# Kernel optimization log

Hardware: AMD Instinct MI355X
Metric: run time of the kernel (lower is better)

The kernel has to match this reference:

```python
import jax, jax.numpy as jnp
import numpy as np

N = 50000
E = 1600000
IN_CH = 128
HID = 32
HEADS = 4
OUT_CH = 64
NEG_SLOPE = 0.2


def _seg_softmax(e, seg, n):
    # e: [E,H], seg: [E] destination indices -> per-destination softmax
    m = jax.ops.segment_max(e, seg, num_segments=n)          # [N,H]
    ex = jnp.exp(e - m[seg])
    s = jax.ops.segment_sum(ex, seg, num_segments=n)         # [N,H]
    return ex / (s[seg] + 1e-16)


def _gat_conv(x, edge_index, W, a_src, a_dst, b, concat):
    # x: [N,Fin]; W: [Fin, H*C]; a_src/a_dst: [H,C]; b: [H*C] or [C]
    H, C = a_src.shape
    n = x.shape[0]
    h = (x @ W).reshape(n, H, C)                              # [N,H,C]
    src, dst = edge_index[0], edge_index[1]
    as_ = jnp.einsum('nhc,hc->nh', h, a_src)                  # [N,H]
    ad_ = jnp.einsum('nhc,hc->nh', h, a_dst)
    e = jax.nn.leaky_relu(as_[src] + ad_[dst], NEG_SLOPE)     # [E,H]
    alpha = _seg_softmax(e, dst, n)                           # [E,H]
    msg = h[src] * alpha[:, :, None]                          # [E,H,C]
    out = jax.ops.segment_sum(msg, dst, num_segments=n)       # [N,H,C]
    out = out.reshape(n, H * C) if concat else out.mean(axis=1)
    return out + b, alpha


def _layer_norm(x, w, b, eps=1e-5):
    mu = x.mean(-1, keepdims=True)
    var = x.var(-1, keepdims=True)
    return (x - mu) * jax.lax.rsqrt(var + eps) * w + b


def setup_inputs() -> dict:
    key = jax.random.key(0)
    ks = jax.random.split(key, 20)
    g = lambda k, s: jax.random.normal(k, s, dtype=jnp.float32) * 0.05
    d = {
        'x': jax.random.normal(ks[0], (N, IN_CH), dtype=jnp.float32),
        'edge_index': jax.random.randint(ks[1], (2, E), 0, N, dtype=jnp.int64),
        # gat1: in=IN_CH, out=HID, heads, concat
        'W1': g(ks[2], (IN_CH, HEADS * HID)),
        'a_src1': g(ks[3], (HEADS, HID)),
        'a_dst1': g(ks[4], (HEADS, HID)),
        'b1': jnp.zeros((HEADS * HID,), jnp.float32),
        'ln1_w': jnp.ones((HEADS * HID,), jnp.float32),
        'ln1_b': jnp.zeros((HEADS * HID,), jnp.float32),
        'Wskip': g(ks[5], (IN_CH, HEADS * HID)),
        'bskip': jnp.zeros((HEADS * HID,), jnp.float32),
        # gat2: in=HEADS*HID, out=HID, concat
        'W2': g(ks[6], (HEADS * HID, HEADS * HID)),
        'a_src2': g(ks[7], (HEADS, HID)),
        'a_dst2': g(ks[8], (HEADS, HID)),
        'b2': jnp.zeros((HEADS * HID,), jnp.float32),
        'ln2_w': jnp.ones((HEADS * HID,), jnp.float32),
        'ln2_b': jnp.zeros((HEADS * HID,), jnp.float32),
        # gat3: in=HEADS*HID, out=OUT_CH, concat=False (mean over heads)
        'W3': g(ks[9], (HEADS * HID, HEADS * OUT_CH)),
        'a_src3': g(ks[10], (HEADS, OUT_CH)),
        'a_dst3': g(ks[11], (HEADS, OUT_CH)),
        'b3': jnp.zeros((OUT_CH,), jnp.float32),
    }
    return d


def reference(x, edge_index, W1, a_src1, a_dst1, b1, ln1_w, ln1_b,
              Wskip, bskip, W2, a_src2, a_dst2, b2, ln2_w, ln2_b,
              W3, a_src3, a_dst3, b3):
    x_skip = x
    h, alpha1 = _gat_conv(x, edge_index, W1, a_src1, a_dst1, b1, concat=True)
    h = jax.nn.elu(h)
    h = _layer_norm(h, ln1_w, ln1_b)
    h = h + (x_skip @ Wskip + bskip)
    h, alpha2 = _gat_conv(h, edge_index, W2, a_src2, a_dst2, b2, concat=True)
    h = jax.nn.elu(h)
    h = _layer_norm(h, ln2_w, ln2_b)
    out, alpha3 = _gat_conv(h, edge_index, W3, a_src3, a_dst3, b3, concat=False)
    return out, alpha1, alpha2, alpha3
```

## Files before the change

### kernel.cpp

```cpp
#include <hip/hip_runtime.h>

#define NN 50000
#define EE 1600000
#define SCAN_B 196
#define NB 196
#define CHUNK 2048
#define G1 782
#define L1 (NB * G1)
#define B1 599

typedef __attribute__((ext_vector_type(8))) short bf16x8;
typedef __attribute__((ext_vector_type(4))) float f32x4;
typedef __attribute__((ext_vector_type(2))) float f32x2;

#if __has_builtin(__builtin_elementwise_fma)
#define PKFMA(a, b, c) __builtin_elementwise_fma((a), (b), (c))
#else
#define PKFMA(a, b, c) ((a) * (b) + (c))
#endif

__device__ __forceinline__ float bfu(unsigned short u) { return __uint_as_float((unsigned)u << 16); }
__device__ __forceinline__ float bflo(unsigned u) { return __uint_as_float(u << 16); }
__device__ __forceinline__ float bfhi(unsigned u) { return __uint_as_float(u & 0xffff0000u); }
__device__ __forceinline__ f32x2 bfpk(unsigned u) {
    f32x2 r; r.x = bflo(u); r.y = bfhi(u); return r;
}
__device__ __forceinline__ unsigned short f2bf(float f) {
    unsigned u = __float_as_uint(f);
    u += 0x7fff + ((u >> 16) & 1);
    return (unsigned short)(u >> 16);
}
__device__ __forceinline__ unsigned pk2(float a, float b) {
    return (unsigned)f2bf(a) | ((unsigned)f2bf(b) << 16);
}
__device__ __forceinline__ float cvt_load(const void* p, int i, bool f32) {
    if (f32) return ((const float*)p)[i];
    return bfu(((const unsigned short*)p)[i]);
}

__global__ void detect_k(const void* ei_raw, const void* x_raw, int* flags) {
    __shared__ int s_i64, s_f32;
    const int t = threadIdx.x;
    if (t == 0) { s_i64 = 1; s_f32 = 0; }
    __syncthreads();
    const int* ei32 = (const int*)ei_raw;
    if (ei32[2 * t + 1] != 0) atomicAnd(&s_i64, 0);
    const unsigned short* xu = (const unsigned short*)x_raw;
    int found = 0;
    for (int j = 0; j < 32; j++) {
        unsigned short u = xu[t * 32 + j];
        if ((u & 0x7F80) == 0x7F80) found = 1;
    }
    if (found) atomicOr(&s_f32, 1);
    __syncthreads();
    if (t == 0) { flags[0] = s_i64; flags[1] = s_f32; }
}

__global__ __launch_bounds__(256) void hist1_k(const void* ei_raw, const int* flags,
                                               int2* __restrict__ edges, int* __restrict__ cnt)
{
    __shared__ int h[NB];
    const int t = threadIdx.x;
    const int i64 = __builtin_amdgcn_readfirstlane(flags[0]);
    if (t < NB) h[t] = 0;
    __syncthreads();
    const int beg = blockIdx.x * CHUNK;
    const int end = min(beg + CHUNK, EE);
    for (int e = beg + t; e < end; e += 256) {
        int2 v;
        if (i64) { const long long* p = (const long long*)ei_raw; v.x = (int)p[e]; v.y = (int)p[EE + e]; }
        else     { const int* p = (const int*)ei_raw;             v.x = p[e];      v.y = p[EE + e];      }
        edges[e] = v;
        atomicAdd(&h[v.y >> 8], 1);
    }
    __syncthreads();
    if (t < NB) cnt[(size_t)t * G1 + blockIdx.x] = h[t];
}

__global__ __launch_bounds__(256) void scanAg_k(int* __restrict__ cnt, int* __restrict__ bsum2) {
    __shared__ int ps[256];
    const int b = blockIdx.x, t = threadIdx.x;
    const int i = b * 256 + t;
    const int v = (i < L1) ? cnt[i] : 0;
    ps[t] = v;
    __syncthreads();
    for (int off = 1; off < 256; off <<= 1) {
        const int u = (t >= off) ? ps[t - off] : 0;
        __syncthreads();
        ps[t] += u;
        __syncthreads();
    }
    if (i < L1) cnt[i] = ps[t] - v;
    if (t == 255) bsum2[b] = ps[255];
}
__global__ void scanBg_k(int* bsum2) {
    __shared__ int ps[256];
    const int t = threadIdx.x;
    int vals[3];
    int s = 0;
    #pragma unroll
    for (int i = 0; i < 3; i++) {
        const int idx = t * 3 + i;
        vals[i] = (idx < B1) ? bsum2[idx] : 0;
        s += vals[i];
    }
    ps[t] = s;
    __syncthreads();
    for (int off = 1; off < 256; off <<= 1) {
        const int u = (t >= off) ? ps[t - off] : 0;
        __syncthreads();
        ps[t] += u;
        __syncthreads();
    }
    int run = t ? ps[t - 1] : 0;
    #pragma unroll
    for (int i = 0; i < 3; i++) {
        const int idx = t * 3 + i;
        if (idx < B1) bsum2[idx] = run;
        run += vals[i];
    }
}
__global__ __launch_bounds__(256) void scanCg_k(int* __restrict__ cnt, const int* __restrict__ bsum2,
                                                int* __restrict__ bstart) {
    const int i = blockIdx.x * 256 + threadIdx.x;
    if (i < L1) {
        const int r = cnt[i] + bsum2[blockIdx.x];
        cnt[i] = r;
        if (i % G1 == 0) bstart[i / G1] = r;
    }
    if (i == 0) bstart[NB] = EE;
}

__global__ __launch_bounds__(256) void scatter_k(const int2* __restrict__ edges,
                                                 const int* __restrict__ cnt,
                                                 int2* __restrict__ bedges)
{
    __shared__ int ofs[NB];
    const int t = threadIdx.x;
    if (t < NB) ofs[t] = cnt[(size_t)t * G1 + blockIdx.x];
    __syncthreads();
    const int beg = blockIdx.x * CHUNK;
    const int end = min(beg + CHUNK, EE);
    for (int e = beg + t; e < end; e += 256) {
        const int2 v = edges[e];
        const int p = atomicAdd(&ofs[v.y >> 8], 1);
        bedges[p] = v;
    }
}

__global__ __launch_bounds__(256) void hist_k(const int2* __restrict__ bedges,
                                              const int* __restrict__ bstart, int* __restrict__ deg)
{
    __shared__ int h[256];
    const int b = blockIdx.x, t = threadIdx.x;
    h[t] = 0;
    __syncthreads();
    const int lo = bstart[b], hi = bstart[b + 1];
    for (int i = lo + t; i < hi; i += 256)
        atomicAdd(&h[bedges[i].y & 255], 1);
    __syncthreads();
    const int d = b * 256 + t;
    if (d < NN) deg[d] = h[t];
}

__global__ __launch_bounds__(256) void scanA_k(const int* __restrict__ deg,
                                               int* __restrict__ roff, int* __restrict__ bsum) {
    __shared__ int ps[256];
    const int b = blockIdx.x, t = threadIdx.x;
    const int i = b * 256 + t;
    const int v = (i < NN) ? deg[i] : 0;
    ps[t] = v;
    __syncthreads();
    for (int off = 1; off < 256; off <<= 1) {
        const int u = (t >= off) ? ps[t - off] : 0;
        __syncthreads();
        ps[t] += u;
        __syncthreads();
    }
    if (i < NN) roff[i] = ps[t] - v;
    if (t == 255) bsum[b] = ps[255];
}
__global__ void scanB_k(int* bsum) {
    __shared__ int ps[256];
    const int t = threadIdx.x;
    const int v = (t < SCAN_B) ? bsum[t] : 0;
    ps[t] = v;
    __syncthreads();
    for (int off = 1; off < 256; off <<= 1) {
        const int u = (t >= off) ? ps[t - off] : 0;
        __syncthreads();
        ps[t] += u;
        __syncthreads();
    }
    if (t < SCAN_B) bsum[t] = ps[t] - v;
}
__global__ __launch_bounds__(256) void scanC_k(int* __restrict__ roff, const int* __restrict__ bsum) {
    const int b = blockIdx.x, t = threadIdx.x;
    const int i = b * 256 + t;
    if (i < NN) roff[i] += bsum[b];
}

__global__ __launch_bounds__(256) void place_k(const int2* __restrict__ bedges,
                                               const int* __restrict__ bstart, const int* __restrict__ roff,
                                               int* __restrict__ csrc)
{
    __shared__ int cur[256];
    const int b = blockIdx.x, t = threadIdx.x;
    const int d = b * 256 + t;
    cur[t] = (d < NN) ? roff[d] : 0;
    __syncthreads();
    const int lo = bstart[b], hi = bstart[b + 1];
    for (int i = lo + t; i < hi; i += 256) {
        const int2 v = bedges[i];
        const int p = atomicAdd(&cur[v.y & 255], 1);
        csrc[p] = v.x;
    }
}

__global__ __launch_bounds__(256) void cvt_all_k(
    const void* x, const void* W1, const void* Wskip, const void* W2, const void* W3,
    const void* as1, const void* ad1, const void* b1, const void* l1w, const void* l1b,
    const void* bsk, const void* as2, const void* ad2, const void* b2, const void* l2w,
    const void* l2b, const void* as3, const void* ad3, const void* b3,
    unsigned short* xb, unsigned short* Wt1, unsigned short* Wts, unsigned short* Wt2,
    unsigned short* Wt3, float* smalls, const int* flags)
{
    const bool f32 = __builtin_amdgcn_readfirstlane(flags[1]) != 0;
    const int gid = blockIdx.x * 256 + threadIdx.x;
    if (gid < NN * 128) { xb[gid] = f2bf(cvt_load(x, gid, f32)); return; }
    int g = gid - NN * 128;
    if (g < 16384) { Wt1[g] = f2bf(cvt_load(W1,    (g & 127) * 128 + (g >> 7), f32)); return; }
    g -= 16384;
    if (g < 16384) { Wts[g] = f2bf(cvt_load(Wskip, (g & 127) * 128 + (g >> 7), f32)); return; }
    g -= 16384;
    if (g < 16384) { Wt2[g] = f2bf(cvt_load(W2,    (g & 127) * 128 + (g >> 7), f32)); return; }
    g -= 16384;
    if (g < 32768) { Wt3[g] = f2bf(cvt_load(W3,    (g & 127) * 256 + (g >> 7), f32)); return; }
    g -= 32768;
    if (g >= 2432) return;
    const void* src; int off;
    if      (g < 128)  { src = as1; off = g;        }
    else if (g < 256)  { src = ad1; off = g - 128;  }
    else if (g < 384)  { src = b1;  off = g - 256;  }
    else if (g < 512)  { src = l1w; off = g - 384;  }
    else if (g < 640)  { src = l1b; off = g - 512;  }
    else if (g < 768)  { src = bsk; off = g - 640;  }
    else if (g < 896)  { src = as2; off = g - 768;  }
    else if (g < 1024) { src = ad2; off = g - 896;  }
    else if (g < 1152) { src = b2;  off = g - 1024; }
    else if (g < 1280) { src = l2w; off = g - 1152; }
    else if (g < 1408) { src = l2b; off = g - 1280; }
    else if (g < 1664) { src = as3; off = g - 1408; }
    else if (g < 1920) { src = ad3; off = g - 1664; }
    else               { src = b3;  off = g - 1920; }
    smalls[g] = cvt_load(src, off, f32);
}

__global__ void prep_v_k(const unsigned short* __restrict__ Wt3, const float* __restrict__ as3,
                         const float* __restrict__ ad3, float* __restrict__ vsrc, float* __restrict__ vdst)
{
    const int t = blockIdx.x * 256 + threadIdx.x;
    if (t >= 512) return;
    const int h = t >> 7, k = t & 127;
    float ss = 0.f, dd = 0.f;
    for (int c = 0; c < 64; c++) {
        const float w = bfu(Wt3[(size_t)(h * 64 + c) * 128 + k]);
        ss = fmaf(w, as3[h * 64 + c], ss);
        dd = fmaf(w, ad3[h * 64 + c], dd);
    }
    vsrc[t] = ss; vdst[t] = dd;
}

template<int FOUT, bool DOTS>
__global__ __launch_bounds__(256) void mfma_mm_k(
    const unsigned short* __restrict__ Xb, const unsigned short* __restrict__ Wt,
    unsigned short* __restrict__ Hb,
    const float* __restrict__ asrc, const float* __restrict__ adst,
    float* __restrict__ as_, float* __restrict__ dpk)
{
    constexpr int NT = FOUT / 16;
    const int tile = blockIdx.x * 4 + (threadIdx.x >> 6);
    if (tile >= 3125) return;
    const int l = threadIdx.x & 63;
    const int lr = l & 15, lq = l >> 4;
    const int m0 = tile * 16;
    f32x4 acc[NT];
    #pragma unroll
    for (int nt = 0; nt < NT; nt++) { acc[nt][0]=0.f; acc[nt][1]=0.f; acc[nt][2]=0.f; acc[nt][3]=0.f; }
    #pragma unroll
    for (int kb = 0; kb < 4; kb++) {
        const bf16x8 a = *(const bf16x8*)(Xb + (size_t)(m0 + lr) * 128 + kb * 32 + lq * 8);
        #pragma unroll
        for (int nt = 0; nt < NT; nt++) {
            const bf16x8 b = *(const bf16x8*)(Wt + (size_t)(nt * 16 + lr) * 128 + kb * 32 + lq * 8);
            acc[nt] = __builtin_amdgcn_mfma_f32_16x16x32_bf16(a, b, acc[nt], 0, 0, 0);
        }
    }
    #pragma unroll
    for (int nt = 0; nt < NT; nt++)
        #pragma unroll
        for (int r = 0; r < 4; r++)
            Hb[(size_t)(m0 + lq * 4 + r) * FOUT + nt * 16 + lr] = f2bf(acc[nt][r]);
    if (DOTS) {
        #pragma unroll
        for (int hd = 0; hd < 4; hd++) {
            const float a0 = asrc[hd * 32 + lr], a1 = asrc[hd * 32 + 16 + lr];
            const float d0 = adst[hd * 32 + lr], d1 = adst[hd * 32 + 16 + lr];
            #pragma unroll
            for (int r = 0; r < 4; r++) {
                float ps = acc[2 * hd][r] * a0 + acc[2 * hd + 1][r] * a1;
                float pd = acc[2 * hd][r] * d0 + acc[2 * hd + 1][r] * d1;
                #pragma unroll
                for (int m = 8; m; m >>= 1) { ps += __shfl_xor(ps, m); pd += __shfl_xor(pd, m); }
                if (lr == 0) {
                    const int node = m0 + lq * 4 + r;
                    as_[(size_t)node * 4 + hd] = ps;
                    dpk[(size_t)node * 8 + hd] = pd;
                }
            }
        }
    }
}

__global__ __launch_bounds__(256) void mm12_k(
    const unsigned short* __restrict__ Xb, const unsigned short* __restrict__ Wt1,
    unsigned short* __restrict__ Hb, unsigned short* __restrict__ Sb,
    const float* __restrict__ asrc, const float* __restrict__ adst,
    float* __restrict__ as_, float* __restrict__ dpk)
{
    const int tile = blockIdx.x * 4 + (threadIdx.x >> 6);
    if (tile >= 3125) return;
    const int l = threadIdx.x & 63;
    const int lr = l & 15, lq = l >> 4;
    const int m0 = tile * 16;
    f32x4 acc[16];
    #pragma unroll
    for (int nt = 0; nt < 16; nt++) { acc[nt][0]=0.f; acc[nt][1]=0.f; acc[nt][2]=0.f; acc[nt][3]=0.f; }
    #pragma unroll
    for (int kb = 0; kb < 4; kb++) {
        const bf16x8 a = *(const bf16x8*)(Xb + (size_t)(m0 + lr) * 128 + kb * 32 + lq * 8);
        #pragma unroll
        for (int nt = 0; nt < 16; nt++) {
            const bf16x8 b = *(const bf16x8*)(Wt1 + (size_t)(nt * 16 + lr) * 128 + kb * 32 + lq * 8);
            acc[nt] = __builtin_amdgcn_mfma_f32_16x16x32_bf16(a, b, acc[nt], 0, 0, 0);
        }
    }
    #pragma unroll
    for (int nt = 0; nt < 8; nt++)
        #pragma unroll
        for (int r = 0; r < 4; r++)
            Hb[(size_t)(m0 + lq * 4 + r) * 128 + nt * 16 + lr] = f2bf(acc[nt][r]);
    #pragma unroll
    for (int nt = 8; nt < 16; nt++)
        #pragma unroll
        for (int r = 0; r < 4; r++)
            Sb[(size_t)(m0 + lq * 4 + r) * 128 + (nt - 8) * 16 + lr] = f2bf(acc[nt][r]);
    #pragma unroll
    for (int hd = 0; hd < 4; hd++) {
        const float a0 = asrc[hd * 32 + lr], a1 = asrc[hd * 32 + 16 + lr];
        const float d0 = adst[hd * 32 + lr], d1 = adst[hd * 32 + 16 + lr];
        #pragma unroll
        for (int r = 0; r < 4; r++) {
            float ps = acc[2 * hd][r] * a0 + acc[2 * hd + 1][r] * a1;
            float pd = acc[2 * hd][r] * d0 + acc[2 * hd + 1][r] * d1;
            #pragma unroll
            for (int m = 8; m; m >>= 1) { ps += __shfl_xor(ps, m); pd += __shfl_xor(pd, m); }
            if (lr == 0) {
                const int node = m0 + lq * 4 + r;
                as_[(size_t)node * 4 + hd] = ps;
                dpk[(size_t)node * 8 + hd] = pd;
            }
        }
    }
}

__device__ __forceinline__ float4 edge_w(float4 as4, float4 ad4) {
    float4 e4;
    e4.x = as4.x + ad4.x; e4.y = as4.y + ad4.y; e4.z = as4.z + ad4.z; e4.w = as4.w + ad4.w;
    e4.x = e4.x >= 0.f ? e4.x : 0.2f * e4.x;
    e4.y = e4.y >= 0.f ? e4.y : 0.2f * e4.y;
    e4.z = e4.z >= 0.f ? e4.z : 0.2f * e4.z;
    e4.w = e4.w >= 0.f ? e4.w : 0.2f * e4.w;
    float4 w4;
    w4.x = __expf(e4.x); w4.y = __expf(e4.y); w4.z = __expf(e4.z); w4.w = __expf(e4.w);
    return w4;
}

template<bool HAS_SKIP, bool DOTS3>
__global__ __launch_bounds__(256) void fagg12_k(
    const int* __restrict__ roff, const int* __restrict__ deg,
    const int* __restrict__ csrc, const float* __restrict__ as_, float* __restrict__ dpk,
    const unsigned short* __restrict__ Hb,
    const float* __restrict__ b, const float* __restrict__ lnw, const float* __restrict__ lnb,
    const unsigned short* __restrict__ skipb, const float* __restrict__ bskip,
    unsigned short* __restrict__ xoutb,
    const float* __restrict__ vsrc, const float* __restrict__ vdst,
    float* __restrict__ as3o, float* __restrict__ dpk3o)
{
    __shared__ float lws[4][512];
    const int warp = threadIdx.x >> 6;
    const int lane = threadIdx.x & 63;
    const int node = blockIdx.x * 4 + warp;
    const int q = lane & 15, g = lane >> 4;
    const int h = q >> 2;
    float* lw = lws[warp];
    const int ro = roff[node], dg = deg[node];
    const float4 ad4 = *(const float4*)(dpk + (size_t)node * 8);

    float4 sv = make_float4(0.f, 0.f, 0.f, 0.f);
    f32x2 acc2[4];
    #pragma unroll
    for (int i = 0; i < 4; i++) { acc2[i].x = 0.f; acc2[i].y = 0.f; }

    for (int j0 = 0; j0 < dg; j0 += 64) {
        const int jn = min(64, dg - j0);
        int src = 0;
        float4 w4 = make_float4(0.f, 0.f, 0.f, 0.f);
        if (lane < jn) {
            src = csrc[ro + j0 + lane];
            const float4 as4 = *(const float4*)(as_ + (size_t)src * 4);
            w4 = edge_w(as4, ad4);
            sv.x += w4.x; sv.y += w4.y; sv.z += w4.z; sv.w += w4.w;
        }
        const float sf = __int_as_float(src);
        *(float4*)(lw + lane * 8)     = make_float4(w4.x, sf, w4.y, sf);
        *(float4*)(lw + lane * 8 + 4) = make_float4(w4.z, sf, w4.w, sf);
        const int jq = (jn + 3) >> 2;
        #pragma unroll 2
        for (int j = 0; j < jq; j++) {
            const int e = 4 * j + g;
            const float2 rd = *(const float2*)(lw + e * 8 + h * 2);
            f32x2 ww; ww.x = rd.x; ww.y = rd.x;
            const unsigned soff = (__float_as_uint(rd.y) << 8) + (unsigned)(q << 4);
            const uint4 hv = *(const uint4*)((const char*)Hb + soff);
            acc2[0] = PKFMA(ww, bfpk(hv.x), acc2[0]);
            acc2[1] = PKFMA(ww, bfpk(hv.y), acc2[1]);
            acc2[2] = PKFMA(ww, bfpk(hv.z), acc2[2]);
            acc2[3] = PKFMA(ww, bfpk(hv.w), acc2[3]);
        }
    }

    #pragma unroll
    for (int i = 0; i < 4; i++) {
        acc2[i].x += __shfl_xor(acc2[i].x, 16);
        acc2[i].y += __shfl_xor(acc2[i].y, 16);
        acc2[i].x += __shfl_xor(acc2[i].x, 32);
        acc2[i].y += __shfl_xor(acc2[i].y, 32);
    }
    #pragma unroll
    for (int m = 32; m; m >>= 1) {
        sv.x += __shfl_xor(sv.x, m); sv.y += __shfl_xor(sv.y, m);
        sv.z += __shfl_xor(sv.z, m); sv.w += __shfl_xor(sv.w, m);
    }
    float4 rs;
    rs.x = 1.f / (sv.x + 1e-16f); rs.y = 1.f / (sv.y + 1e-16f);
    rs.z = 1.f / (sv.z + 1e-16f); rs.w = 1.f / (sv.w + 1e-16f);
    if (lane == 0) *(float4*)(dpk + (size_t)node * 8 + 4) = rs;
    const float rsh = (h == 0) ? rs.x : (h == 1) ? rs.y : (h == 2) ? rs.z : rs.w;

    const float4 b0 = *(const float4*)(b + q * 8);
    const float4 b1 = *(const float4*)(b + q * 8 + 4);
    float v[8];
    v[0] = acc2[0].x * rsh + b0.x; v[1] = acc2[0].y * rsh + b0.y;
    v[2] = acc2[1].x * rsh + b0.z; v[3] = acc2[1].y * rsh + b0.w;
    v[4] = acc2[2].x * rsh + b1.x; v[5] = acc2[2].y * rsh + b1.y;
    v[6] = acc2[3].x * rsh + b1.z; v[7] = acc2[3].y * rsh + b1.w;
    float s1 = 0.f, s2 = 0.f;
    #pragma unroll
    for (int i = 0; i < 8; i++) {
        v[i] = v[i] > 0.f ? v[i] : expm1f(v[i]);
        s1 += v[i]; s2 += v[i] * v[i];
    }
    #pragma unroll
    for (int m = 8; m; m >>= 1) { s1 += __shfl_xor(s1, m); s2 += __shfl_xor(s2, m); }
    const float mu   = s1 * (1.f / 128.f);
    const float var  = s2 * (1.f / 128.f) - mu * mu;
    const float rstd = rsqrtf(var + 1e-5f);
    const float4 w0 = *(const float4*)(lnw + q * 8);
    const float4 w1 = *(const float4*)(lnw + q * 8 + 4);
    const float4 o0 = *(const float4*)(lnb + q * 8);
    const float4 o1 = *(const float4*)(lnb + q * 8 + 4);
    float y[8];
    y[0] = (v[0] - mu) * rstd * w0.x + o0.x; y[1] = (v[1] - mu) * rstd * w0.y + o0.y;
    y[2] = (v[2] - mu) * rstd * w0.z + o0.z; y[3] = (v[3] - mu) * rstd * w0.w + o0.w;
    y[4] = (v[4] - mu) * rstd * w1.x + o1.x; y[5] = (v[5] - mu) * rstd * w1.y + o1.y;
    y[6] = (v[6] - mu) * rstd * w1.z + o1.z; y[7] = (v[7] - mu) * rstd * w1.w + o1.w;
    if (HAS_SKIP) {
        const uint4 sk = *(const uint4*)(skipb + (size_t)node * 128 + q * 8);
        const float4 k0 = *(const float4*)(bskip + q * 8);
        const float4 k1 = *(const float4*)(bskip + q * 8 + 4);
        y[0] += bflo(sk.x) + k0.x; y[1] += bfhi(sk.x) + k0.y;
        y[2] += bflo(sk.y) + k0.z; y[3] += bfhi(sk.y) + k0.w;
        y[4] += bflo(sk.z) + k1.x; y[5] += bfhi(sk.z) + k1.y;
        y[6] += bflo(sk.w) + k1.z; y[7] += bfhi(sk.w) + k1.w;
    }
    if (g == 0) {
        uint4 pk;
        pk.x = pk2(y[0], y[1]); pk.y = pk2(y[2], y[3]);
        pk.z = pk2(y[4], y[5]); pk.w = pk2(y[6], y[7]);
        *(uint4*)(xoutb + (size_t)node * 128 + q * 8) = pk;
    }
    if (DOTS3) {
        #pragma unroll
        for (int hd = 0; hd < 4; hd++) {
            const float4 vs0 = *(const float4*)(vsrc + hd * 128 + q * 8);
            const float4 vs1 = *(const float4*)(vsrc + hd * 128 + q * 8 + 4);
            const float4 vd0 = *(const float4*)(vdst + hd * 128 + q * 8);
            const float4 vd1 = *(const float4*)(vdst + hd * 128 + q * 8 + 4);
            float ss = y[0] * vs0.x + y[1] * vs0.y + y[2] * vs0.z + y[3] * vs0.w
                     + y[4] * vs1.x + y[5] * vs1.y + y[6] * vs1.z + y[7] * vs1.w;
            float dd = y[0] * vd0.x + y[1] * vd0.y + y[2] * vd0.z + y[3] * vd0.w
                     + y[4] * vd1.x + y[5] * vd1.y + y[6] * vd1.z + y[7] * vd1.w;
            #pragma unroll
            for (int m = 8; m; m >>= 1) { ss += __shfl_xor(ss, m); dd += __shfl_xor(dd, m); }
            if (lane == 0) {
                as3o[(size_t)node * 4 + hd] = ss;
                dpk3o[(size_t)node * 8 + hd] = dd;
            }
        }
    }
}

__global__ __launch_bounds__(256) void fagg3_k(
    const int* __restrict__ roff, const int* __restrict__ deg,
    const int* __restrict__ csrc, const float* __restrict__ as_, float* __restrict__ dpk,
    const unsigned short* __restrict__ Xb,
    unsigned short* __restrict__ gout)
{
    __shared__ float lws[4][256];
    __shared__ int lss[4][64];
    const int warp = threadIdx.x >> 6;
    const int lane = threadIdx.x & 63;
    const int node = blockIdx.x * 4 + warp;
    const int q = lane & 31, g = lane >> 5;
    float* lw = lws[warp];
    int*   ls = lss[warp];
    const int ro = roff[node], dg = deg[node];
    const float4 ad4 = *(const float4*)(dpk + (size_t)node * 8);

    float4 sv = make_float4(0.f, 0.f, 0.f, 0.f);
    f32x2 acc2[4][2];
    #pragma unroll
    for (int hh = 0; hh < 4; hh++)
        #pragma unroll
        for (int i = 0; i < 2; i++) { acc2[hh][i].x = 0.f; acc2[hh][i].y = 0.f; }

    for (int j0 = 0; j0 < dg; j0 += 64) {
        const int jn = min(64, dg - j0);
        int src = 0;
        float4 w4 = make_float4(0.f, 0.f, 0.f, 0.f);
        if (lane < jn) {
            src = csrc[ro + j0 + lane];
            const float4 as4 = *(const float4*)(as_ + (size_t)src * 4);
            w4 = edge_w(as4, ad4);
            sv.x += w4.x; sv.y += w4.y; sv.z += w4.z; sv.w += w4.w;
        }
        *(float4*)(lw + lane * 4) = w4;
        ls[lane] = src;
        const int jq = (jn + 1) >> 1;
        #pragma unroll 2
        for (int j = 0; j < jq; j++) {
            const int e = 2 * j + g;
            const float4 w = *(const float4*)(lw + e * 4);
            const int s_ = ls[e];
            const unsigned soff = ((unsigned)s_ << 8) + (unsigned)(q << 3);
            const uint2 hv = *(const uint2*)((const char*)Xb + soff);
            const f32x2 x01 = bfpk(hv.x), x23 = bfpk(hv.y);
            f32x2 w0; w0.x = w.x; w0.y = w.x;
            f32x2 w1; w1.x = w.y; w1.y = w.y;
            f32x2 w2; w2.x = w.z; w2.y = w.z;
            f32x2 w3; w3.x = w.w; w3.y = w.w;
            acc2[0][0] = PKFMA(w0, x01, acc2[0][0]); acc2[0][1] = PKFMA(w0, x23, acc2[0][1]);
            acc2[1][0] = PKFMA(w1, x01, acc2[1][0]); acc2[1][1] = PKFMA(w1, x23, acc2[1][1]);
            acc2[2][0] = PKFMA(w2, x01, acc2[2][0]); acc2[2][1] = PKFMA(w2, x23, acc2[2][1]);
            acc2[3][0] = PKFMA(w3, x01, acc2[3][0]); acc2[3][1] = PKFMA(w3, x23, acc2[3][1]);
        }
    }

    #pragma unroll
    for (int hh = 0; hh < 4; hh++)
        #pragma unroll
        for (int i = 0; i < 2; i++) {
            acc2[hh][i].x += __shfl_xor(acc2[hh][i].x, 32);
            acc2[hh][i].y += __shfl_xor(acc2[hh][i].y, 32);
        }
    #pragma unroll
    for (int m = 32; m; m >>= 1) {
        sv.x += __shfl_xor(sv.x, m); sv.y += __shfl_xor(sv.y, m);
        sv.z += __shfl_xor(sv.z, m); sv.w += __shfl_xor(sv.w, m);
    }
    float4 rs;
    rs.x = 1.f / (sv.x + 1e-16f); rs.y = 1.f / (sv.y + 1e-16f);
    rs.z = 1.f / (sv.z + 1e-16f); rs.w = 1.f / (sv.w + 1e-16f);
    if (lane == 0) *(float4*)(dpk + (size_t)node * 8 + 4) = rs;

    unsigned short* gr = gout + (size_t)node * 512 + 4 * q;
    if (g == 0) {
        uint2 p0, p1;
        p0.x = pk2(acc2[0][0].x * rs.x, acc2[0][0].y * rs.x);
        p0.y = pk2(acc2[0][1].x * rs.x, acc2[0][1].y * rs.x);
        p1.x = pk2(acc2[1][0].x * rs.y, acc2[1][0].y * rs.y);
        p1.y = pk2(acc2[1][1].x * rs.y, acc2[1][1].y * rs.y);
        *(uint2*)(gr)       = p0;
        *(uint2*)(gr + 128) = p1;
    } else {
        uint2 p2, p3;
        p2.x = pk2(acc2[2][0].x * rs.z, acc2[2][0].y * rs.z);
        p2.y = pk2(acc2[2][1].x * rs.z, acc2[2][1].y * rs.z);
        p3.x = pk2(acc2[3][0].x * rs.w, acc2[3][0].y * rs.w);
        p3.y = pk2(acc2[3][1].x * rs.w, acc2[3][1].y * rs.w);
        *(uint2*)(gr + 256) = p2;
        *(uint2*)(gr + 384) = p3;
    }
}

__global__ __launch_bounds__(256) void alpha_l_k(
    const int2* __restrict__ edges, const float* __restrict__ as_,
    const float* __restrict__ dpk, float* __restrict__ al)
{
    const int e = blockIdx.x * 256 + threadIdx.x;
    const int2 v = edges[e];
    const float4 as4 = *(const float4*)(as_ + (size_t)v.x * 4);
    const float4 ad4 = *(const float4*)(dpk + (size_t)v.y * 8);
    const float4 r   = *(const float4*)(dpk + (size_t)v.y * 8 + 4);
    const float4 w = edge_w(as4, ad4);
    float4 a; a.x = w.x * r.x; a.y = w.y * r.y; a.z = w.z * r.z; a.w = w.w * r.w;
    *(float4*)(al + (size_t)e * 4) = a;
}

__global__ __launch_bounds__(256) void proj3_k(
    const unsigned short* __restrict__ Gb, const unsigned short* __restrict__ Wt3,
    const float* __restrict__ b3, float* __restrict__ out)
{
    const int tile = blockIdx.x * 4 + (threadIdx.x >> 6);
    if (tile >= 3125) return;
    const int l = threadIdx.x & 63;
    const int lr = l & 15, lq = l >> 4;
    const int m0 = tile * 16;
    f32x4 acc[4];
    #pragma unroll
    for (int nt = 0; nt < 4; nt++) { acc[nt][0]=0.f; acc[nt][1]=0.f; acc[nt][2]=0.f; acc[nt][3]=0.f; }
    #pragma unroll
    for (int kb = 0; kb < 16; kb++) {
        const int h = kb >> 2;
        const int kk = (kb & 3) * 32 + lq * 8;
        const bf16x8 a = *(const bf16x8*)(Gb + (size_t)(m0 + lr) * 512 + kb * 32 + lq * 8);
        #pragma unroll
        for (int nt = 0; nt < 4; nt++) {
            const int c = nt * 16 + lr;
            const bf16x8 b = *(const bf16x8*)(Wt3 + (size_t)(h * 64 + c) * 128 + kk);
            acc[nt] = __builtin_amdgcn_mfma_f32_16x16x32_bf16(a, b, acc[nt], 0, 0, 0);
        }
    }
    #pragma unroll
    for (int nt = 0; nt < 4; nt++)
        #pragma unroll
        for (int r = 0; r < 4; r++) {
            const int col = nt * 16 + lr;
            out[(size_t)(m0 + lq * 4 + r) * 64 + col] = 0.25f * acc[nt][r] + b3[col];
        }
}

extern "C" void kernel_launch(void* const* d_in, const int* in_sizes, int n_in,
                              void* d_out, int out_size, void* d_ws, size_t ws_size,
                              hipStream_t stream)
{
    char* ws = (char*)d_ws;
    unsigned short* g_bf    = (unsigned short*)(ws);
    int2*           bedges  = (int2*)(ws);
    int*            csrc    = (int*)(ws + 51200000);
    unsigned short* x_bf    = (unsigned short*)(ws + 57600000);
    unsigned short* xcur_bf = (unsigned short*)(ws + 70400000);
    unsigned short* skip_bf = (unsigned short*)(ws + 83200000);
    unsigned short* Hbuf    = (unsigned short*)(ws + 96000000);
    int2*  edges  = (int2*)(ws + 108800000);
    float* as1b   = (float*)(ws + 121600000);
    float* as2b   = as1b + 200000;
    float* as3b   = as1b + 400000;
    float* dpk1   = as1b + 600000;
    float* dpk2   = as1b + 1000000;
    float* dpk3   = as1b + 1400000;
    int*   roff   = (int*)(ws + 128800000);
    int*   deg    = (int*)(ws + 129000000);
    int*   bsum   = (int*)(ws + 129200000);
    int*   flags  = (int*)(ws + 129402048);
    unsigned short* Wt1 = (unsigned short*)(ws + 129500000);
    unsigned short* Wts = Wt1 + 16384;
    unsigned short* Wt2 = Wts + 16384;
    unsigned short* Wt3 = Wt2 + 16384;
    float* smalls = (float*)(ws + 129700000);
    float* vsrc   = (float*)(ws + 129720000);
    float* vdst   = (float*)(ws + 129730000);
    int*   cnt    = (int*)(ws + 130000000);
    int*   bsum2  = (int*)(ws + 130700000);
    int*   bstart = (int*)(ws + 130710000);

    float* as1c = smalls;          float* ad1c = smalls + 128;
    float* b1c  = smalls + 256;    float* l1wc = smalls + 384;
    float* l1bc = smalls + 512;    float* bskc = smalls + 640;
    float* as2c = smalls + 768;    float* ad2c = smalls + 896;
    float* b2c  = smalls + 1024;   float* l2wc = smalls + 1152;
    float* l2bc = smalls + 1280;   float* as3c = smalls + 1408;
    float* ad3c = smalls + 1664;   float* b3c  = smalls + 1920;

    float* out = (float*)d_out;
    float* al1 = out + (size_t)NN * 64;
    float* al2 = al1 + (size_t)EE * 4;
    float* al3 = al2 + (size_t)EE * 4;

    detect_k<<<1, 256, 0, stream>>>(d_in[1], d_in[0], flags);
    hist1_k<<<G1, 256, 0, stream>>>(d_in[1], flags, edges, cnt);
    cvt_all_k<<<25330, 256, 0, stream>>>(
        d_in[0], d_in[2], d_in[8], d_in[10], d_in[16],
        d_in[3], d_in[4], d_in[5], d_in[6], d_in[7],
        d_in[9], d_in[11], d_in[12], d_in[13], d_in[14], d_in[15],
        d_in[17], d_in[18], d_in[19],
        x_bf, Wt1, Wts, Wt2, Wt3, smalls, flags);
    scanAg_k<<<B1, 256, 0, stream>>>(cnt, bsum2);
    scanBg_k<<<1, 256, 0, stream>>>(bsum2);
    scanCg_k<<<B1, 256, 0, stream>>>(cnt, bsum2, bstart);
    scatter_k<<<G1, 256, 0, stream>>>(edges, cnt, bedges);
    hist_k<<<NB, 256, 0, stream>>>(bedges, bstart, deg);
    scanA_k<<<SCAN_B, 256, 0, stream>>>(deg, roff, bsum);
    scanB_k<<<1, 256, 0, stream>>>(bsum);
    scanC_k<<<SCAN_B, 256, 0, stream>>>(roff, bsum);
    place_k<<<NB, 256, 0, stream>>>(bedges, bstart, roff, csrc);
    prep_v_k<<<2, 256, 0, stream>>>(Wt3, as3c, ad3c, vsrc, vdst);

    mm12_k<<<782, 256, 0, stream>>>(x_bf, Wt1, Hbuf, skip_bf, as1c, ad1c, as1b, dpk1);
    fagg12_k<true, false><<<12500, 256, 0, stream>>>(roff, deg, csrc, as1b, dpk1, Hbuf,
                                                     b1c, l1wc, l1bc, skip_bf, bskc, xcur_bf,
                                                     nullptr, nullptr, nullptr, nullptr);

    mfma_mm_k<128, true><<<782, 256, 0, stream>>>(xcur_bf, Wt2, Hbuf, as2c, ad2c, as2b, dpk2);
    fagg12_k<false, true><<<12500, 256, 0, stream>>>(roff, deg, csrc, as2b, dpk2, Hbuf,
                                                     b2c, l2wc, l2bc, nullptr, nullptr, xcur_bf,
                                                     vsrc, vdst, as3b, dpk3);

    fagg3_k<<<12500, 256, 0, stream>>>(roff, deg, csrc, as3b, dpk3, xcur_bf, g_bf);
    proj3_k<<<782, 256, 0, stream>>>(g_bf, Wt3, b3c, out);

    alpha_l_k<<<6250, 256, 0, stream>>>(edges, as1b, dpk1, al1);
    alpha_l_k<<<6250, 256, 0, stream>>>(edges, as2b, dpk2, al2);
    alpha_l_k<<<6250, 256, 0, stream>>>(edges, as3b, dpk3, al3);
}
```

Before: 580.2 us.

## Process two destination nodes per wavefront in aggregation kernels

The three aggregation kernels now split each 64-lane wavefront into two 32-lane halves, each handling its own destination node. Edge chunks shrink to 32 and the grid is halved. With an average degree of about 32, fewer lanes sit idle and the cross-half shuffle reductions disappear. The ELU also swaps expm1f for __expf minus one, which trades a little accuracy near zero for cheaper math.

```diff
diff --git a/kernel.cpp b/kernel.cpp
--- a/kernel.cpp
+++ b/kernel.cpp
@@ -400,10 +400,12 @@
     __shared__ float lws[4][512];
     const int warp = threadIdx.x >> 6;
     const int lane = threadIdx.x & 63;
-    const int node = blockIdx.x * 4 + warp;
-    const int q = lane & 15, g = lane >> 4;
+    const int half = lane >> 5;
+    const int l32  = lane & 31;
+    const int node = blockIdx.x * 8 + warp * 2 + half;
+    const int q = l32 & 15, g = l32 >> 4;
     const int h = q >> 2;
-    float* lw = lws[warp];
+    float* lw = lws[warp] + half * 256;
     const int ro = roff[node], dg = deg[node];
     const float4 ad4 = *(const float4*)(dpk + (size_t)node * 8);
 
@@ -412,23 +414,23 @@
     #pragma unroll
     for (int i = 0; i < 4; i++) { acc2[i].x = 0.f; acc2[i].y = 0.f; }
 
-    for (int j0 = 0; j0 < dg; j0 += 64) {
-        const int jn = min(64, dg - j0);
+    for (int j0 = 0; j0 < dg; j0 += 32) {
+        const int jn = min(32, dg - j0);
         int src = 0;
         float4 w4 = make_float4(0.f, 0.f, 0.f, 0.f);
-        if (lane < jn) {
-            src = csrc[ro + j0 + lane];
+        if (l32 < jn) {
+            src = csrc[ro + j0 + l32];
             const float4 as4 = *(const float4*)(as_ + (size_t)src * 4);
             w4 = edge_w(as4, ad4);
             sv.x += w4.x; sv.y += w4.y; sv.z += w4.z; sv.w += w4.w;
         }
         const float sf = __int_as_float(src);
-        *(float4*)(lw + lane * 8)     = make_float4(w4.x, sf, w4.y, sf);
-        *(float4*)(lw + lane * 8 + 4) = make_float4(w4.z, sf, w4.w, sf);
-        const int jq = (jn + 3) >> 2;
+        *(float4*)(lw + l32 * 8)     = make_float4(w4.x, sf, w4.y, sf);
+        *(float4*)(lw + l32 * 8 + 4) = make_float4(w4.z, sf, w4.w, sf);
+        const int jq = (jn + 1) >> 1;
         #pragma unroll 2
         for (int j = 0; j < jq; j++) {
-            const int e = 4 * j + g;
+            const int e = 2 * j + g;
             const float2 rd = *(const float2*)(lw + e * 8 + h * 2);
             f32x2 ww; ww.x = rd.x; ww.y = rd.x;
             const unsigned soff = (__float_as_uint(rd.y) << 8) + (unsigned)(q << 4);
@@ -444,18 +446,16 @@
     for (int i = 0; i < 4; i++) {
         acc2[i].x += __shfl_xor(acc2[i].x, 16);
         acc2[i].y += __shfl_xor(acc2[i].y, 16);
-        acc2[i].x += __shfl_xor(acc2[i].x, 32);
-        acc2[i].y += __shfl_xor(acc2[i].y, 32);
-    }
-    #pragma unroll
-    for (int m = 32; m; m >>= 1) {
+    }
+    #pragma unroll
+    for (int m = 16; m; m >>= 1) {
         sv.x += __shfl_xor(sv.x, m); sv.y += __shfl_xor(sv.y, m);
         sv.z += __shfl_xor(sv.z, m); sv.w += __shfl_xor(sv.w, m);
     }
     float4 rs;
     rs.x = 1.f / (sv.x + 1e-16f); rs.y = 1.f / (sv.y + 1e-16f);
     rs.z = 1.f / (sv.z + 1e-16f); rs.w = 1.f / (sv.w + 1e-16f);
-    if (lane == 0) *(float4*)(dpk + (size_t)node * 8 + 4) = rs;
+    if (l32 == 0) *(float4*)(dpk + (size_t)node * 8 + 4) = rs;
     const float rsh = (h == 0) ? rs.x : (h == 1) ? rs.y : (h == 2) ? rs.z : rs.w;
 
     const float4 b0 = *(const float4*)(b + q * 8);
@@ -468,7 +468,7 @@
     float s1 = 0.f, s2 = 0.f;
     #pragma unroll
     for (int i = 0; i < 8; i++) {
-        v[i] = v[i] > 0.f ? v[i] : expm1f(v[i]);
+        v[i] = v[i] > 0.f ? v[i] : (__expf(v[i]) - 1.f);
         s1 += v[i]; s2 += v[i] * v[i];
     }
     #pragma unroll
@@ -513,7 +513,7 @@
                      + y[4] * vd1.x + y[5] * vd1.y + y[6] * vd1.z + y[7] * vd1.w;
             #pragma unroll
             for (int m = 8; m; m >>= 1) { ss += __shfl_xor(ss, m); dd += __shfl_xor(dd, m); }
-            if (lane == 0) {
+            if (l32 == 0) {
                 as3o[(size_t)node * 4 + hd] = ss;
                 dpk3o[(size_t)node * 8 + hd] = dd;
             }
@@ -531,10 +531,11 @@
     __shared__ int lss[4][64];
     const int warp = threadIdx.x >> 6;
     const int lane = threadIdx.x & 63;
-    const int node = blockIdx.x * 4 + warp;
-    const int q = lane & 31, g = lane >> 5;
-    float* lw = lws[warp];
-    int*   ls = lss[warp];
+    const int half = lane >> 5;
+    const int l32  = lane & 31;
+    const int node = blockIdx.x * 8 + warp * 2 + half;
+    float* lw = lws[warp] + half * 128;
+    int*   ls = lss[warp] + half * 32;
     const int ro = roff[node], dg = deg[node];
     const float4 ad4 = *(const float4*)(dpk + (size_t)node * 8);
 
@@ -545,25 +546,22 @@
         #pragma unroll
         for (int i = 0; i < 2; i++) { acc2[hh][i].x = 0.f; acc2[hh][i].y = 0.f; }
 
-    for (int j0 = 0; j0 < dg; j0 += 64) {
-        const int jn = min(64, dg - j0);
+    for (int j0 = 0; j0 < dg; j0 += 32) {
+        const int jn = min(32, dg - j0);
         int src = 0;
         float4 w4 = make_float4(0.f, 0.f, 0.f, 0.f);
-        if (lane < jn) {
-            src = csrc[ro + j0 + lane];
+        if (l32 < jn) {
+            src = csrc[ro + j0 + l32];
             const float4 as4 = *(const float4*)(as_ + (size_t)src * 4);
             w4 = edge_w(as4, ad4);
             sv.x += w4.x; sv.y += w4.y; sv.z += w4.z; sv.w += w4.w;
         }
-        *(float4*)(lw + lane * 4) = w4;
-        ls[lane] = src;
-        const int jq = (jn + 1) >> 1;
-        #pragma unroll 2
-        for (int j = 0; j < jq; j++) {
-            const int e = 2 * j + g;
-            const float4 w = *(const float4*)(lw + e * 4);
-            const int s_ = ls[e];
-            const unsigned soff = ((unsigned)s_ << 8) + (unsigned)(q << 3);
+        *(float4*)(lw + l32 * 4) = w4;
+        ls[l32] = src;
+        for (int j = 0; j < jn; j++) {
+            const float4 w = *(const float4*)(lw + j * 4);
+            const int s_ = ls[j];
+            const unsigned soff = ((unsigned)s_ << 8) + (unsigned)(l32 << 3);
             const uint2 hv = *(const uint2*)((const char*)Xb + soff);
             const f32x2 x01 = bfpk(hv.x), x23 = bfpk(hv.y);
             f32x2 w0; w0.x = w.x; w0.y = w.x;
@@ -578,40 +576,29 @@
     }
 
     #pragma unroll
-    for (int hh = 0; hh < 4; hh++)
-        #pragma unroll
-        for (int i = 0; i < 2; i++) {
-            acc2[hh][i].x += __shfl_xor(acc2[hh][i].x, 32);
-            acc2[hh][i].y += __shfl_xor(acc2[hh][i].y, 32);
-        }
-    #pragma unroll
-    for (int m = 32; m; m >>= 1) {
+    for (int m = 16; m; m >>= 1) {
         sv.x += __shfl_xor(sv.x, m); sv.y += __shfl_xor(sv.y, m);
         sv.z += __shfl_xor(sv.z, m); sv.w += __shfl_xor(sv.w, m);
     }
     float4 rs;
     rs.x = 1.f / (sv.x + 1e-16f); rs.y = 1.f / (sv.y + 1e-16f);
     rs.z = 1.f / (sv.z + 1e-16f); rs.w = 1.f / (sv.w + 1e-16f);
-    if (lane == 0) *(float4*)(dpk + (size_t)node * 8 + 4) = rs;
-
-    unsigned short* gr = gout + (size_t)node * 512 + 4 * q;
-    if (g == 0) {
-        uint2 p0, p1;
-        p0.x = pk2(acc2[0][0].x * rs.x, acc2[0][0].y * rs.x);
-        p0.y = pk2(acc2[0][1].x * rs.x, acc2[0][1].y * rs.x);
-        p1.x = pk2(acc2[1][0].x * rs.y, acc2[1][0].y * rs.y);
-        p1.y = pk2(acc2[1][1].x * rs.y, acc2[1][1].y * rs.y);
-        *(uint2*)(gr)       = p0;
-        *(uint2*)(gr + 128) = p1;
-    } else {
-        uint2 p2, p3;
-        p2.x = pk2(acc2[2][0].x * rs.z, acc2[2][0].y * rs.z);
-        p2.y = pk2(acc2[2][1].x * rs.z, acc2[2][1].y * rs.z);
-        p3.x = pk2(acc2[3][0].x * rs.w, acc2[3][0].y * rs.w);
-        p3.y = pk2(acc2[3][1].x * rs.w, acc2[3][1].y * rs.w);
-        *(uint2*)(gr + 256) = p2;
-        *(uint2*)(gr + 384) = p3;
-    }
+    if (l32 == 0) *(float4*)(dpk + (size_t)node * 8 + 4) = rs;
+
+    unsigned short* gr = gout + (size_t)node * 512 + 4 * l32;
+    uint2 p0, p1, p2, p3;
+    p0.x = pk2(acc2[0][0].x * rs.x, acc2[0][0].y * rs.x);
+    p0.y = pk2(acc2[0][1].x * rs.x, acc2[0][1].y * rs.x);
+    p1.x = pk2(acc2[1][0].x * rs.y, acc2[1][0].y * rs.y);
+    p1.y = pk2(acc2[1][1].x * rs.y, acc2[1][1].y * rs.y);
+    p2.x = pk2(acc2[2][0].x * rs.z, acc2[2][0].y * rs.z);
+    p2.y = pk2(acc2[2][1].x * rs.z, acc2[2][1].y * rs.z);
+    p3.x = pk2(acc2[3][0].x * rs.w, acc2[3][0].y * rs.w);
+    p3.y = pk2(acc2[3][1].x * rs.w, acc2[3][1].y * rs.w);
+    *(uint2*)(gr)       = p0;
+    *(uint2*)(gr + 128) = p1;
+    *(uint2*)(gr + 256) = p2;
+    *(uint2*)(gr + 384) = p3;
 }
 
 __global__ __launch_bounds__(256) void alpha_l_k(
@@ -728,16 +715,16 @@
     prep_v_k<<<2, 256, 0, stream>>>(Wt3, as3c, ad3c, vsrc, vdst);
 
     mm12_k<<<782, 256, 0, stream>>>(x_bf, Wt1, Hbuf, skip_bf, as1c, ad1c, as1b, dpk1);
-    fagg12_k<true, false><<<12500, 256, 0, stream>>>(roff, deg, csrc, as1b, dpk1, Hbuf,
-                                                     b1c, l1wc, l1bc, skip_bf, bskc, xcur_bf,
-                                                     nullptr, nullptr, nullptr, nullptr);
+    fagg12_k<true, false><<<6250, 256, 0, stream>>>(roff, deg, csrc, as1b, dpk1, Hbuf,
+                                                    b1c, l1wc, l1bc, skip_bf, bskc, xcur_bf,
+                                                    nullptr, nullptr, nullptr, nullptr);
 
     mfma_mm_k<128, true><<<782, 256, 0, stream>>>(xcur_bf, Wt2, Hbuf, as2c, ad2c, as2b, dpk2);
-    fagg12_k<false, true><<<12500, 256, 0, stream>>>(roff, deg, csrc, as2b, dpk2, Hbuf,
-                                                     b2c, l2wc, l2bc, nullptr, nullptr, xcur_bf,
-                                                     vsrc, vdst, as3b, dpk3);
-
-    fagg3_k<<<12500, 256, 0, stream>>>(roff, deg, csrc, as3b, dpk3, xcur_bf, g_bf);
+    fagg12_k<false, true><<<6250, 256, 0, stream>>>(roff, deg, csrc, as2b, dpk2, Hbuf,
+                                                    b2c, l2wc, l2bc, nullptr, nullptr, xcur_bf,
+                                                    vsrc, vdst, as3b, dpk3);
+
+    fagg3_k<<<6250, 256, 0, stream>>>(roff, deg, csrc, as3b, dpk3, xcur_bf, g_bf);
     proj3_k<<<782, 256, 0, stream>>>(g_bf, Wt3, b3c, out);
 
     alpha_l_k<<<6250, 256, 0, stream>>>(edges, as1b, dpk1, al1);
```

Measured after the change: 570.2 us. No clear change (-1.7%).
